# Optimization experiments

Measured on AMD Instinct MI355X. Metric: run time of the kernel, lower is better.

Reference implementation:

```python
import jax, jax.numpy as jnp
import numpy as np

B, S, E = 512, 200, 128
NUM_C = 1024
DIFF = 100


def _glorot(k, shape):
    fan_in, fan_out = shape[-1], shape[0]
    lim = jnp.sqrt(6.0 / (fan_in + fan_out)).astype(jnp.float32)
    return jax.random.uniform(k, shape, jnp.float32, -lim, lim)


def setup_inputs() -> dict:
    key = jax.random.key(0)
    ks = jax.random.split(key, 16)
    c = jax.random.randint(ks[0], (B, S), 0, NUM_C + 1)
    sd = jax.random.randint(ks[1], (B, S), 0, DIFF + 2)
    a = jax.random.randint(ks[2], (B, S), 0, 2)
    cshft = jax.random.randint(ks[3], (B, S), 0, NUM_C + 1)
    sdshft = jax.random.randint(ks[4], (B, S), 0, DIFF + 2)
    # embedding tables (padding_idx=0 rows zeroed, as in nn.Embedding)
    c_table = _glorot(ks[5], (NUM_C + 1, E)).at[0].set(0.0)
    sd_table = _glorot(ks[6], (DIFF + 2, E)).at[0].set(0.0)
    a_table = _glorot(ks[7], (2, E))
    knowledge = _glorot(ks[8], (1, E))  # xavier_uniform [1, E]
    W1 = _glorot(ks[9], (E, 2 * E)); b1 = jnp.zeros((E,), jnp.float32)
    W2 = _glorot(ks[10], (E, E));     b2 = jnp.zeros((E,), jnp.float32)
    W3 = _glorot(ks[11], (E, E));     b3 = jnp.zeros((E,), jnp.float32)
    W4 = _glorot(ks[12], (E, 2 * E)); b4 = jnp.zeros((E,), jnp.float32)
    W5 = _glorot(ks[13], (E, 2 * E)); b5 = jnp.zeros((E,), jnp.float32)
    W6 = _glorot(ks[14], (E, 3 * E)); b6 = jnp.zeros((E,), jnp.float32)
    return dict(c=c, sd=sd, a=a, cshft=cshft, sdshft=sdshft,
                c_table=c_table, sd_table=sd_table, a_table=a_table,
                knowledge=knowledge,
                W1=W1, b1=b1, W2=W2, b2=b2, W3=W3, b3=b3,
                W4=W4, b4=b4, W5=W5, b5=b5, W6=W6, b6=b6)


def reference(c, sd, a, cshft, sdshft, c_table, sd_table, a_table, knowledge,
              W1, b1, W2, b2, W3, b3, W4, b4, W5, b5, W6, b6):
    # embedding lookups: [B, S, E]
    c_emb = c_table[c]
    sd_emb = sd_table[sd]
    a_emb = a_table[a]
    target_c = c_table[cshft]
    target_sd = sd_table[sdshft]

    input_data = jnp.concatenate((c_emb, sd_emb), -1) @ W1.T + b1      # [B,S,E]
    target_data = jnp.concatenate((target_c, target_sd), -1) @ W1.T + b1

    k0 = jnp.broadcast_to(knowledge, (c.shape[0], knowledge.shape[-1]))  # [B,E]

    def step(k, xs):
        sd_t, a_t, in_t = xs                       # each [B,E]
        qq = k - in_t
        gates_SDF = jax.nn.sigmoid(qq @ W2.T + b2)
        SDFt = gates_SDF * jnp.tanh(qq @ W3.T + b3)  # dropout = eval-mode identity
        x = jnp.concatenate((SDFt, a_t), -1)
        gates_PKA = jax.nn.sigmoid(x @ W4.T + b4)
        PKAt = gates_PKA * jnp.tanh(x @ W5.T + b5)
        ins = jnp.concatenate((k, a_t, sd_t), -1)
        gates_KSU = jax.nn.sigmoid(ins @ W6.T + b6)
        k_new = gates_KSU * k + (1.0 - gates_KSU) * PKAt
        return k_new, k_new

    xs = (jnp.swapaxes(sd_emb, 0, 1),      # [S,B,E]
          jnp.swapaxes(a_emb, 0, 1),
          jnp.swapaxes(input_data, 0, 1))
    _, hs = jax.lax.scan(step, k0, xs)     # hs: [S,B,E]
    output = jnp.swapaxes(hs, 0, 1)        # [B,S,E]

    logits = jnp.sum(target_data * output, axis=-1)  # [B,S]
    return jax.nn.sigmoid(logits)
```

## Files before the change

### kernel.cpp

```cpp
#include <hip/hip_runtime.h>


#define S_ 200
#define E_ 128
#define RS 136

typedef float  float4v __attribute__((ext_vector_type(4)));
typedef _Float16 f16x8 __attribute__((ext_vector_type(8)));

#define BAR() asm volatile("s_waitcnt lgkmcnt(0)\n\ts_barrier" ::: "memory")

__device__ __forceinline__ float fast_sigmoid(float x) {
  return __builtin_amdgcn_rcpf(1.f + __expf(-x));
}
__device__ __forceinline__ float fast_tanh(float x) {
  return 2.f * __builtin_amdgcn_rcpf(1.f + __expf(-2.f * x)) - 1.f;
}

#define DPP_ADD(x, ctrl) \
  ((x) + __builtin_bit_cast(float, __builtin_amdgcn_update_dpp( \
       0, __builtin_bit_cast(int, (x)), (ctrl), 0xf, 0xf, true)))

__device__ __forceinline__ f16x8 cvt8(const float* __restrict__ p) {
  float4v a = *(const float4v*)p;
  float4v b = *(const float4v*)(p + 4);
  f16x8 r;
  r[0] = (_Float16)a[0]; r[1] = (_Float16)a[1];
  r[2] = (_Float16)a[2]; r[3] = (_Float16)a[3];
  r[4] = (_Float16)b[0]; r[5] = (_Float16)b[1];
  r[6] = (_Float16)b[2]; r[7] = (_Float16)b[3];
  return r;
}

__global__ __launch_bounds__(256) void dimkt_prep(
    const float* __restrict__ c_table, const float* __restrict__ sd_table,
    const float* __restrict__ a_table,
    const float* __restrict__ W1, const float* __restrict__ b1,
    const float* __restrict__ W4, const float* __restrict__ b4,
    const float* __restrict__ W5, const float* __restrict__ b5,
    const float* __restrict__ W6, const float* __restrict__ b6,
    float* __restrict__ ws) {
  __shared__ __attribute__((aligned(16))) float s_src[8][E_];
  __shared__ float s_w[E_][33];
  const int blk = blockIdx.x, t = threadIdx.x;
  const int e = t & 127, h = t >> 7;
  const float* src; const float* wb; const float* bias; float* dst;
  int r0, maxrow, wstr, woff;
  if (blk < 129)      { r0 = blk * 8;       src = c_table;  maxrow = 1024; wb = W1; wstr = 256; woff = 0;   bias = nullptr; dst = ws; }
  else if (blk < 142) { r0 = (blk-129) * 8; src = sd_table; maxrow = 101;  wb = W1; wstr = 256; woff = 128; bias = b1;      dst = ws + 131200; }
  else if (blk < 155) { r0 = (blk-142) * 8; src = sd_table; maxrow = 101;  wb = W6; wstr = 384; woff = 256; bias = nullptr; dst = ws + 144256; }
  else if (blk == 155){ r0 = 0;             src = a_table;  maxrow = 1;    wb = W4; wstr = 256; woff = 128; bias = b4;      dst = ws + 157312; }
  else if (blk == 156){ r0 = 0;             src = a_table;  maxrow = 1;    wb = W5; wstr = 256; woff = 128; bias = b5;      dst = ws + 157568; }
  else                { r0 = 0;             src = a_table;  maxrow = 1;    wb = W6; wstr = 384; woff = 128; bias = b6;      dst = ws + 157824; }
  #pragma unroll
  for (int i = 0; i < 4; ++i) {
    int idx = i * 256 + t, row = idx >> 7, col = idx & 127;
    int rr = r0 + row; if (rr > maxrow) rr = maxrow;
    s_src[row][col] = src[rr * E_ + col];
  }
  float binit = bias ? bias[e] : 0.f;
  float acc[4] = {binit, binit, binit, binit};
  for (int k0 = 0; k0 < 4; ++k0) {
    __syncthreads();
    #pragma unroll
    for (int i = 0; i < 16; ++i) {
      int idx = i * 256 + t;
      s_w[idx >> 5][idx & 31] = wb[(idx >> 5) * wstr + woff + k0 * 32 + (idx & 31)];
    }
    __syncthreads();
    #pragma unroll 4
    for (int kk = 0; kk < 32; ++kk) {
      float wv = s_w[e][kk];
      #pragma unroll
      for (int g = 0; g < 4; ++g)
        acc[g] += wv * s_src[h * 4 + g][k0 * 32 + kk];
    }
  }
  #pragma unroll
  for (int g = 0; g < 4; ++g) {
    int row = r0 + h * 4 + g;
    if (row <= maxrow) dst[row * E_ + e] = acc[g];
  }
}

__global__ __launch_bounds__(512, 2) void dimkt_scan(
    const int* __restrict__ c, const int* __restrict__ sd, const int* __restrict__ a,
    const int* __restrict__ cshft, const int* __restrict__ sdshft,
    const float* __restrict__ knowledge,
    const float* __restrict__ W2, const float* __restrict__ b2,
    const float* __restrict__ W3, const float* __restrict__ b3,
    const float* __restrict__ W4, const float* __restrict__ W5,
    const float* __restrict__ W6,
    const float* __restrict__ ws, float* __restrict__ out) {

  const float* __restrict__ C1  = ws;
  const float* __restrict__ SD1 = ws + 131200;
  const float* __restrict__ SD6 = ws + 144256;
  const float* __restrict__ A4  = ws + 157312;
  const float* __restrict__ A5  = ws + 157568;
  const float* __restrict__ A6  = ws + 157824;

  const int tid  = threadIdx.x;
  const int w    = tid >> 6;
  const int lane = tid & 63;
  const int l15  = lane & 15;
  const int q    = lane >> 4;
  const int qodd = q & 1;
  const int e    = w * 16 + l15;
  const int j    = q >> 1;
  const int bj   = blockIdx.x * 2 + j;

  __shared__ __attribute__((aligned(16))) _Float16 A1[16 * RS];
  __shared__ __attribute__((aligned(16))) _Float16 A2[16 * RS];
  __shared__ __attribute__((aligned(32))) int idx_lds[S_][2][8];
  __shared__ float part[8][2][S_];

  for (int i = tid; i < 2 * S_; i += 512) {
    const int jj = (i >= S_) ? 1 : 0;
    const int ss = jj ? (i - S_) : i;
    const int src = (blockIdx.x * 2 + jj) * S_ + ss;
    idx_lds[ss][jj][0] = c[src];
    idx_lds[ss][jj][1] = sd[src];
    idx_lds[ss][jj][2] = a[src];
    idx_lds[ss][jj][3] = cshft[src];
    idx_lds[ss][jj][4] = sdshft[src];
  }

  const int stq = (j * 8) * RS + e;
  const int stk = stq + RS;
  const int rd0 = l15 * RS + q * 8;
  const bool m1 = (l15 & 6) == 0;
  const bool m2 = (l15 & 7) == 0;

  f16x8 w2f[4], w3f[4], w4f[4], w5f[4], w6f[4];
  #pragma unroll
  for (int t = 0; t < 4; ++t) {
    const int ko = t * 32 + q * 8;
    w2f[t] = cvt8(W2 + e * 128 + ko);
    w3f[t] = cvt8(W3 + e * 128 + ko);
    w4f[t] = cvt8(W4 + e * 256 + ko);
    w5f[t] = cvt8(W5 + e * 256 + ko);
    w6f[t] = cvt8(W6 + e * 384 + ko);
  }
  const float b2e = b2[e], b3e = b3[e];
  const float A4t0 = A4[e], A4t1 = A4[E_ + e];
  const float A5t0 = A5[e], A5t1 = A5[E_ + e];
  const float A6t0 = A6[e], A6t1 = A6[E_ + e];

  float kreg = knowledge[e];

  const int base = bj * S_;
  int ic = c[base], isd = sd[base], ia = a[base], ict = cshft[base], ist = sdshft[base];
  float inT  = C1[ic * E_ + e] + SD1[isd * E_ + e];
  float sd6v = SD6[isd * E_ + e];
  float a4v = ia ? A4t1 : A4t0;
  float a5v = ia ? A5t1 : A5t0;
  float a6v = ia ? A6t1 : A6t0;
  float tgt  = C1[ict * E_ + e] + SD1[ist * E_ + e];
  int nic = c[base + 1], nisd = sd[base + 1], nia = a[base + 1],
      nict = cshft[base + 1], nist = sdshft[base + 1];

  __syncthreads();
  if (!qodd) {
    A1[stq] = (_Float16)(kreg - inT);
    A1[stk] = (_Float16)kreg;
  }
  __syncthreads();

  f16x8 f0{}, f1{}, f2{}, f3{};
  f16x8 g0{}, g1{}, g2v{}, g3{};

  float4v acc2{0.f,0.f,0.f,0.f}, acc3{0.f,0.f,0.f,0.f}, acc6{0.f,0.f,0.f,0.f};
  float4v acc4{0.f,0.f,0.f,0.f}, acc5{0.f,0.f,0.f,0.f};

  float pprev = 0.f;
  int   sprev = 0;

  #pragma unroll 1
  for (int s = 0; s < S_; ++s) {
    if (m1) {
      f0 = *(const f16x8*)&A1[rd0];
      f1 = *(const f16x8*)&A1[rd0 + 32];
      f2 = *(const f16x8*)&A1[rd0 + 64];
      f3 = *(const f16x8*)&A1[rd0 + 96];
    }

    if (s > 0) {
      float pr = pprev;
      pr = DPP_ADD(pr, 0x111);
      pr = DPP_ADD(pr, 0x112);
      pr = DPP_ADD(pr, 0x114);
      pr = DPP_ADD(pr, 0x118);
      if (l15 == 15 && !qodd) part[w][j][sprev] = pr;
    }

    float ninT = C1[nic * E_ + e] + SD1[nisd * E_ + e];
    float nsd6 = SD6[nisd * E_ + e];
    float na4 = nia ? A4t1 : A4t0;
    float na5 = nia ? A5t1 : A5t0;
    float na6 = nia ? A6t1 : A6t0;
    float ntg  = C1[nict * E_ + e] + SD1[nist * E_ + e];

    const int s2 = (s + 2 < S_) ? (s + 2) : (S_ - 1);
    const int4 iv = *(const int4*)&idx_lds[s2][j][0];
    const int tist = idx_lds[s2][j][4];

    acc2[0] = b2e;
    acc3[0] = b3e;
    acc2 = __builtin_amdgcn_mfma_f32_16x16x32_f16(f0, w2f[0], acc2, 0, 0, 0);
    acc3 = __builtin_amdgcn_mfma_f32_16x16x32_f16(f0, w3f[0], acc3, 0, 0, 0);
    acc2 = __builtin_amdgcn_mfma_f32_16x16x32_f16(f1, w2f[1], acc2, 0, 0, 0);
    acc3 = __builtin_amdgcn_mfma_f32_16x16x32_f16(f1, w3f[1], acc3, 0, 0, 0);
    acc2 = __builtin_amdgcn_mfma_f32_16x16x32_f16(f2, w2f[2], acc2, 0, 0, 0);
    acc3 = __builtin_amdgcn_mfma_f32_16x16x32_f16(f2, w3f[2], acc3, 0, 0, 0);
    acc2 = __builtin_amdgcn_mfma_f32_16x16x32_f16(f3, w2f[3], acc2, 0, 0, 0);
    acc3 = __builtin_amdgcn_mfma_f32_16x16x32_f16(f3, w3f[3], acc3, 0, 0, 0);

    acc6[1] = a6v + sd6v;
    acc6 = __builtin_amdgcn_mfma_f32_16x16x32_f16(f0, w6f[0], acc6, 0, 0, 0);
    acc6 = __builtin_amdgcn_mfma_f32_16x16x32_f16(f1, w6f[1], acc6, 0, 0, 0);

    const float g2  = fast_sigmoid(acc2[0]);
    const float th3 = fast_tanh(acc3[0]);
    const float sdfv = g2 * th3;
    if (!qodd) A2[stq] = (_Float16)sdfv;

    acc6 = __builtin_amdgcn_mfma_f32_16x16x32_f16(f2, w6f[2], acc6, 0, 0, 0);
    acc6 = __builtin_amdgcn_mfma_f32_16x16x32_f16(f3, w6f[3], acc6, 0, 0, 0);

    BAR();

    if (m2) {
      g0  = *(const f16x8*)&A2[rd0];
      g1  = *(const f16x8*)&A2[rd0 + 32];
      g2v = *(const f16x8*)&A2[rd0 + 64];
      g3  = *(const f16x8*)&A2[rd0 + 96];
    }

    const float g6 = fast_sigmoid(acc6[1]);

    acc4[0] = a4v;
    acc4 = __builtin_amdgcn_mfma_f32_16x16x32_f16(g0, w4f[0], acc4, 0, 0, 0);
    acc4 = __builtin_amdgcn_mfma_f32_16x16x32_f16(g1, w4f[1], acc4, 0, 0, 0);
    acc4 = __builtin_amdgcn_mfma_f32_16x16x32_f16(g2v, w4f[2], acc4, 0, 0, 0);
    acc4 = __builtin_amdgcn_mfma_f32_16x16x32_f16(g3, w4f[3], acc4, 0, 0, 0);
    acc5[0] = a5v;
    acc5 = __builtin_amdgcn_mfma_f32_16x16x32_f16(g0, w5f[0], acc5, 0, 0, 0);
    acc5 = __builtin_amdgcn_mfma_f32_16x16x32_f16(g1, w5f[1], acc5, 0, 0, 0);

    const float s4 = fast_sigmoid(acc4[0]);

    acc5 = __builtin_amdgcn_mfma_f32_16x16x32_f16(g2v, w5f[2], acc5, 0, 0, 0);
    acc5 = __builtin_amdgcn_mfma_f32_16x16x32_f16(g3, w5f[3], acc5, 0, 0, 0);

    const float t5  = fast_tanh(acc5[0]);
    const float pka = s4 * t5;
    const float knew = pka + g6 * (kreg - pka);
    kreg = knew;
    if (!qodd) {
      A1[stq] = (_Float16)(knew - ninT);
      A1[stk] = (_Float16)knew;
    }

    pprev = tgt * knew;
    sprev = s;

    inT = ninT; sd6v = nsd6; a4v = na4; a5v = na5; a6v = na6; tgt = ntg;
    nic = iv.x; nisd = iv.y; nia = iv.z; nict = iv.w; nist = tist;

    BAR();
  }

  {
    float pr = pprev;
    pr = DPP_ADD(pr, 0x111);
    pr = DPP_ADD(pr, 0x112);
    pr = DPP_ADD(pr, 0x114);
    pr = DPP_ADD(pr, 0x118);
    if (l15 == 15 && !qodd) part[w][j][sprev] = pr;
  }

  __syncthreads();
  for (int i = tid; i < 2 * S_; i += 512) {
    const int jj = (i >= S_) ? 1 : 0;
    const int ss = jj ? (i - S_) : i;
    float logit = 0.f;
    #pragma unroll
    for (int x = 0; x < 8; ++x) logit += part[x][jj][ss];
    out[(blockIdx.x * 2 + jj) * S_ + ss] = fast_sigmoid(logit);
  }
}

extern "C" void kernel_launch(void* const* d_in, const int* in_sizes, int n_in,
                              void* d_out, int out_size, void* d_ws, size_t ws_size,
                              hipStream_t stream) {
  const int*   c         = (const int*)  d_in[0];
  const int*   sd        = (const int*)  d_in[1];
  const int*   a         = (const int*)  d_in[2];
  const int*   cshft     = (const int*)  d_in[3];
  const int*   sdshft    = (const int*)  d_in[4];
  const float* c_table   = (const float*)d_in[5];
  const float* sd_table  = (const float*)d_in[6];
  const float* a_table   = (const float*)d_in[7];
  const float* knowledge = (const float*)d_in[8];
  const float* W1 = (const float*)d_in[9];  const float* b1 = (const float*)d_in[10];
  const float* W2 = (const float*)d_in[11]; const float* b2 = (const float*)d_in[12];
  const float* W3 = (const float*)d_in[13]; const float* b3 = (const float*)d_in[14];
  const float* W4 = (const float*)d_in[15]; const float* b4 = (const float*)d_in[16];
  const float* W5 = (const float*)d_in[17]; const float* b5 = (const float*)d_in[18];
  const float* W6 = (const float*)d_in[19]; const float* b6 = (const float*)d_in[20];
  float* ws  = (float*)d_ws;
  float* out = (float*)d_out;
  (void)in_sizes; (void)n_in; (void)out_size; (void)ws_size;

  dimkt_prep<<<158, 256, 0, stream>>>(c_table, sd_table, a_table,
                                      W1, b1, W4, b4, W5, b5, W6, b6, ws);
  dimkt_scan<<<256, 512, 0, stream>>>(c, sd, a, cshft, sdshft, knowledge,
                                      W2, b2, W3, b3, W4, W5, W6, ws, out);
}
```

Measured before the change: 262.1 us.

## Split MFMA accumulation chains, stage SD tables in LDS, restrict gathers to even quads

Each dependent MFMA accumulation chain is split into two independent accumulators that are summed before the activation. This shortens the serial MFMA latency per recurrent step. The SD1 and SD6 tables are copied into shared memory once per block, and the per-step gathers now read them from LDS and are done only by even quads, with the index prefetch depth cut from two steps to one. The cost is about 104 KB of extra LDS, which can limit occupancy, plus a larger prologue copy.

```diff
diff --git a/kernel.cpp b/kernel.cpp
--- a/kernel.cpp
+++ b/kernel.cpp
@@ -114,6 +114,8 @@
   __shared__ __attribute__((aligned(16))) _Float16 A2[16 * RS];
   __shared__ __attribute__((aligned(32))) int idx_lds[S_][2][8];
   __shared__ float part[8][2][S_];
+  __shared__ __attribute__((aligned(16))) float SD1L[102 * E_];
+  __shared__ __attribute__((aligned(16))) float SD6L[102 * E_];
 
   for (int i = tid; i < 2 * S_; i += 512) {
     const int jj = (i >= S_) ? 1 : 0;
@@ -125,6 +127,10 @@
     idx_lds[ss][jj][3] = cshft[src];
     idx_lds[ss][jj][4] = sdshft[src];
   }
+  for (int i = tid; i < 102 * E_; i += 512) {
+    SD1L[i] = SD1[i];
+    SD6L[i] = SD6[i];
+  }
 
   const int stq = (j * 8) * RS + e;
   const int stk = stq + RS;
@@ -151,18 +157,16 @@
 
   const int base = bj * S_;
   int ic = c[base], isd = sd[base], ia = a[base], ict = cshft[base], ist = sdshft[base];
-  float inT  = C1[ic * E_ + e] + SD1[isd * E_ + e];
+  float inT0 = C1[ic * E_ + e] + SD1[isd * E_ + e];
   float sd6v = SD6[isd * E_ + e];
   float a4v = ia ? A4t1 : A4t0;
   float a5v = ia ? A5t1 : A5t0;
   float a6v = ia ? A6t1 : A6t0;
-  float tgt  = C1[ict * E_ + e] + SD1[ist * E_ + e];
-  int nic = c[base + 1], nisd = sd[base + 1], nia = a[base + 1],
-      nict = cshft[base + 1], nist = sdshft[base + 1];
+  float tgt = C1[ict * E_ + e] + SD1[ist * E_ + e];
 
   __syncthreads();
   if (!qodd) {
-    A1[stq] = (_Float16)(kreg - inT);
+    A1[stq] = (_Float16)(kreg - inT0);
     A1[stk] = (_Float16)kreg;
   }
   __syncthreads();
@@ -170,8 +174,13 @@
   f16x8 f0{}, f1{}, f2{}, f3{};
   f16x8 g0{}, g1{}, g2v{}, g3{};
 
-  float4v acc2{0.f,0.f,0.f,0.f}, acc3{0.f,0.f,0.f,0.f}, acc6{0.f,0.f,0.f,0.f};
-  float4v acc4{0.f,0.f,0.f,0.f}, acc5{0.f,0.f,0.f,0.f};
+  float4v a2a{0.f,0.f,0.f,0.f}, a2b{0.f,0.f,0.f,0.f};
+  float4v a3a{0.f,0.f,0.f,0.f}, a3b{0.f,0.f,0.f,0.f};
+  float4v acc6{0.f,0.f,0.f,0.f};
+  float4v a4a{0.f,0.f,0.f,0.f}, a4b{0.f,0.f,0.f,0.f};
+  float4v a5a{0.f,0.f,0.f,0.f}, a5b{0.f,0.f,0.f,0.f};
+
+  float ninT = 0.f, nsd6 = 0.f, na4 = 0.f, na5 = 0.f, na6 = 0.f, ntg = 0.f;
 
   float pprev = 0.f;
   int   sprev = 0;
@@ -194,34 +203,35 @@
       if (l15 == 15 && !qodd) part[w][j][sprev] = pr;
     }
 
-    float ninT = C1[nic * E_ + e] + SD1[nisd * E_ + e];
-    float nsd6 = SD6[nisd * E_ + e];
-    float na4 = nia ? A4t1 : A4t0;
-    float na5 = nia ? A5t1 : A5t0;
-    float na6 = nia ? A6t1 : A6t0;
-    float ntg  = C1[nict * E_ + e] + SD1[nist * E_ + e];
-
-    const int s2 = (s + 2 < S_) ? (s + 2) : (S_ - 1);
-    const int4 iv = *(const int4*)&idx_lds[s2][j][0];
-    const int tist = idx_lds[s2][j][4];
-
-    acc2[0] = b2e;
-    acc3[0] = b3e;
-    acc2 = __builtin_amdgcn_mfma_f32_16x16x32_f16(f0, w2f[0], acc2, 0, 0, 0);
-    acc3 = __builtin_amdgcn_mfma_f32_16x16x32_f16(f0, w3f[0], acc3, 0, 0, 0);
-    acc2 = __builtin_amdgcn_mfma_f32_16x16x32_f16(f1, w2f[1], acc2, 0, 0, 0);
-    acc3 = __builtin_amdgcn_mfma_f32_16x16x32_f16(f1, w3f[1], acc3, 0, 0, 0);
-    acc2 = __builtin_amdgcn_mfma_f32_16x16x32_f16(f2, w2f[2], acc2, 0, 0, 0);
-    acc3 = __builtin_amdgcn_mfma_f32_16x16x32_f16(f2, w3f[2], acc3, 0, 0, 0);
-    acc2 = __builtin_amdgcn_mfma_f32_16x16x32_f16(f3, w2f[3], acc2, 0, 0, 0);
-    acc3 = __builtin_amdgcn_mfma_f32_16x16x32_f16(f3, w3f[3], acc3, 0, 0, 0);
+    if (!qodd) {
+      const int s1 = (s + 1 < S_) ? (s + 1) : (S_ - 1);
+      const int4 iv = *(const int4*)&idx_lds[s1][j][0];
+      const int ist1 = idx_lds[s1][j][4];
+      ninT = C1[iv.x * E_ + e] + SD1L[iv.y * E_ + e];
+      nsd6 = SD6L[iv.y * E_ + e];
+      na4 = iv.z ? A4t1 : A4t0;
+      na5 = iv.z ? A5t1 : A5t0;
+      na6 = iv.z ? A6t1 : A6t0;
+      ntg  = C1[iv.w * E_ + e] + SD1L[ist1 * E_ + e];
+    }
+
+    a2a[0] = b2e;  a2b[0] = 0.f;
+    a3a[0] = b3e;  a3b[0] = 0.f;
+    a2a = __builtin_amdgcn_mfma_f32_16x16x32_f16(f0, w2f[0], a2a, 0, 0, 0);
+    a3a = __builtin_amdgcn_mfma_f32_16x16x32_f16(f0, w3f[0], a3a, 0, 0, 0);
+    a2b = __builtin_amdgcn_mfma_f32_16x16x32_f16(f1, w2f[1], a2b, 0, 0, 0);
+    a3b = __builtin_amdgcn_mfma_f32_16x16x32_f16(f1, w3f[1], a3b, 0, 0, 0);
+    a2a = __builtin_amdgcn_mfma_f32_16x16x32_f16(f2, w2f[2], a2a, 0, 0, 0);
+    a3a = __builtin_amdgcn_mfma_f32_16x16x32_f16(f2, w3f[2], a3a, 0, 0, 0);
+    a2b = __builtin_amdgcn_mfma_f32_16x16x32_f16(f3, w2f[3], a2b, 0, 0, 0);
+    a3b = __builtin_amdgcn_mfma_f32_16x16x32_f16(f3, w3f[3], a3b, 0, 0, 0);
 
     acc6[1] = a6v + sd6v;
     acc6 = __builtin_amdgcn_mfma_f32_16x16x32_f16(f0, w6f[0], acc6, 0, 0, 0);
     acc6 = __builtin_amdgcn_mfma_f32_16x16x32_f16(f1, w6f[1], acc6, 0, 0, 0);
 
-    const float g2  = fast_sigmoid(acc2[0]);
-    const float th3 = fast_tanh(acc3[0]);
+    const float g2  = fast_sigmoid(a2a[0] + a2b[0]);
+    const float th3 = fast_tanh(a3a[0] + a3b[0]);
     const float sdfv = g2 * th3;
     if (!qodd) A2[stq] = (_Float16)sdfv;
 
@@ -239,34 +249,31 @@
 
     const float g6 = fast_sigmoid(acc6[1]);
 
-    acc4[0] = a4v;
-    acc4 = __builtin_amdgcn_mfma_f32_16x16x32_f16(g0, w4f[0], acc4, 0, 0, 0);
-    acc4 = __builtin_amdgcn_mfma_f32_16x16x32_f16(g1, w4f[1], acc4, 0, 0, 0);
-    acc4 = __builtin_amdgcn_mfma_f32_16x16x32_f16(g2v, w4f[2], acc4, 0, 0, 0);
-    acc4 = __builtin_amdgcn_mfma_f32_16x16x32_f16(g3, w4f[3], acc4, 0, 0, 0);
-    acc5[0] = a5v;
-    acc5 = __builtin_amdgcn_mfma_f32_16x16x32_f16(g0, w5f[0], acc5, 0, 0, 0);
-    acc5 = __builtin_amdgcn_mfma_f32_16x16x32_f16(g1, w5f[1], acc5, 0, 0, 0);
-
-    const float s4 = fast_sigmoid(acc4[0]);
-
-    acc5 = __builtin_amdgcn_mfma_f32_16x16x32_f16(g2v, w5f[2], acc5, 0, 0, 0);
-    acc5 = __builtin_amdgcn_mfma_f32_16x16x32_f16(g3, w5f[3], acc5, 0, 0, 0);
-
-    const float t5  = fast_tanh(acc5[0]);
+    a4a[0] = a4v;  a4b[0] = 0.f;
+    a5a[0] = a5v;  a5b[0] = 0.f;
+    a4a = __builtin_amdgcn_mfma_f32_16x16x32_f16(g0, w4f[0], a4a, 0, 0, 0);
+    a5a = __builtin_amdgcn_mfma_f32_16x16x32_f16(g0, w5f[0], a5a, 0, 0, 0);
+    a4b = __builtin_amdgcn_mfma_f32_16x16x32_f16(g1, w4f[1], a4b, 0, 0, 0);
+    a5b = __builtin_amdgcn_mfma_f32_16x16x32_f16(g1, w5f[1], a5b, 0, 0, 0);
+    a4a = __builtin_amdgcn_mfma_f32_16x16x32_f16(g2v, w4f[2], a4a, 0, 0, 0);
+    a5a = __builtin_amdgcn_mfma_f32_16x16x32_f16(g2v, w5f[2], a5a, 0, 0, 0);
+    a4b = __builtin_amdgcn_mfma_f32_16x16x32_f16(g3, w4f[3], a4b, 0, 0, 0);
+    a5b = __builtin_amdgcn_mfma_f32_16x16x32_f16(g3, w5f[3], a5b, 0, 0, 0);
+
+    const float s4 = fast_sigmoid(a4a[0] + a4b[0]);
+    const float t5 = fast_tanh(a5a[0] + a5b[0]);
     const float pka = s4 * t5;
     const float knew = pka + g6 * (kreg - pka);
     kreg = knew;
     if (!qodd) {
+      A1[stk] = (_Float16)knew;
       A1[stq] = (_Float16)(knew - ninT);
-      A1[stk] = (_Float16)knew;
     }
 
     pprev = tgt * knew;
     sprev = s;
 
-    inT = ninT; sd6v = nsd6; a4v = na4; a5v = na5; a6v = na6; tgt = ntg;
-    nic = iv.x; nisd = iv.y; nia = iv.z; nict = iv.w; nist = tist;
+    sd6v = nsd6; a4v = na4; a5v = na5; a6v = na6; tgt = ntg;
 
     BAR();
   }
```

Result: slower. 279.9 us (+6.8%).
